# Kernel optimization log

Measured on AMD Instinct MI355X. Metric: run time of the kernel, lower is better.

## Reference

```python
import jax, jax.numpy as jnp
import numpy as np

SHOT, WAY, DIM, Q, R = 5, 32, 640, 4096, 10
TEMP, L, DIV = 16.0, 2.0, 10.0
EPS = 1e-5


def _expmap0(x, c):
    # x: (..., d); c: broadcastable to (..., 1). Exponential map at origin + ball projection.
    sc = jnp.sqrt(c)
    n = jnp.maximum(jnp.linalg.norm(x, axis=-1, keepdims=True), EPS)
    y = jnp.tanh(sc * n) * x / (sc * n)
    ny = jnp.maximum(jnp.linalg.norm(y, axis=-1, keepdims=True), EPS)
    maxn = (1.0 - 1e-3) / sc
    return jnp.where(ny > maxn, y * (maxn / ny), y)


def _dist(x, y, c):
    # Poincare distance: 2/sqrt(c) * artanh(sqrt(c) * ||mobius_add(-x, y)||)
    u = -x
    uy = jnp.sum(u * y, -1, keepdims=True)
    u2 = jnp.sum(u * u, -1, keepdims=True)
    y2 = jnp.sum(y * y, -1, keepdims=True)
    num = (1.0 + 2.0 * c * uy + c * y2) * u + (1.0 - c * u2) * y
    den = jnp.maximum(1.0 + 2.0 * c * uy + c * c * u2 * y2, EPS)
    n = jnp.linalg.norm(num / den, axis=-1, keepdims=True)
    sc = jnp.sqrt(c)
    arg = jnp.clip(sc * n, 0.0, 1.0 - EPS)
    return ((2.0 / sc) * jnp.arctanh(arg))[..., 0]


def setup_inputs() -> dict:
    key = jax.random.key(0)
    ks = jax.random.split(key, 8)
    f = lambda k, s: jax.random.normal(k, s, dtype=jnp.float32)
    z = lambda s: jnp.zeros(s, jnp.float32)
    return {
        "data_shot": f(ks[0], (SHOT * WAY, DIM)),
        "data_query": f(ks[1], (Q, DIM)),
        "W1": f(ks[2], (2 * DIM, 128)) * 0.05, "b1": z((128,)),
        "W2": f(ks[3], (128, 64)) * 0.05, "b2": z((64,)),
        "W3": f(ks[4], (64, 5)) * 0.05, "b3": z((5,)),
        "Wr1": f(ks[5], (2 * R + 2, R)) * 0.05, "br1": z((R,)),
        "Wr2": f(ks[6], (R, R + 1)) * 0.05, "br2": z((R + 1,)),
    }


def reference(data_shot, data_query, W1, b1, W2, b2, W3, b3, Wr1, br1, Wr2, br2):
    # --- episode stats + per-class curvature controller ---
    all_data = jnp.concatenate([data_shot, data_query], 0).mean(0)      # (dim,)
    protos = data_shot.reshape(SHOT, WAY, DIM).mean(0)                  # (way, dim)
    ctrl_in = jnp.concatenate([protos, jnp.broadcast_to(all_data, (WAY, DIM))], 1)
    h = jax.nn.relu(ctrl_in @ W1 + b1)
    h = jax.nn.relu(h @ W2 + b2)
    cand = jnp.arange(1, 6, dtype=jnp.float32) * (L / DIV)              # 5 curvature candidates
    c = jax.nn.softmax(h @ W3 + b3, axis=-1) @ cand                     # (way,) positive curvature

    # --- hyperbolic projection + per-class proto-query distances (vectorized over classes) ---
    proto_p = _expmap0(protos, c[:, None])                              # (way, dim)
    query_p = _expmap0(data_query[None], c[:, None, None])              # (way, Q, dim)
    dis_mat = _dist(proto_p[:, None, :], query_p, c[:, None, None])     # (way, Q)

    # --- sort + gather-based rerank features ---
    idx = jnp.argsort(dis_mat, axis=1)
    idx_near, idx_far = idx[:, :R], idx[:, R:]
    n_i_d = jnp.take_along_axis(dis_mat, idx_near, 1)                   # (way, R)
    o_i_d = jnp.take_along_axis(dis_mat, idx_far, 1).mean(1)            # (way,)
    dT = dis_mat.T                                                      # (Q, way)
    Gnear = dT[idx_near]                                                # (way, R, way): [i,k,j] = dis_mat[j, idx_near[i,k]]
    n_o_d = (Gnear.sum(-1) - n_i_d) / (WAY - 1)                         # (way, R)
    Gfar = dT[idx_far]                                                  # (way, Q-R, way)
    ii = jnp.arange(WAY)
    mlt = (ii[None, :] < ii[:, None]).astype(dis_mat.dtype)             # j < i
    mgt = (ii[None, :] > ii[:, None]).astype(dis_mat.dtype)             # j > i
    sumA = jnp.einsum('ikj,ij->i', Gfar, mlt)                           # gathered cols (rows before i)
    sumB = mgt @ dis_mat[:, R:].sum(1)                                  # raw cols R: (rows after i, as in source)
    o_o_d = (sumA + sumB) / ((WAY - 1) * (Q - R))

    # --- rerank controller MLP ---
    rr_in = jnp.concatenate([n_i_d, n_o_d, o_i_d[:, None], o_o_d[:, None]], 1)  # (way, 2R+2)
    hr = jax.nn.relu(rr_in @ Wr1 + br1)
    orr = hr @ Wr2 + br2                                                # (way, R+1)
    i_w = jax.nn.softmax(orr[:, :R], axis=-1)                           # (way, R)
    onw = jax.nn.sigmoid(orr[:, R])                                     # (way,)

    # --- proto update + final distances ---
    near_q = data_query[idx_near]                                       # (way, R, dim)
    wdq = (near_q * i_w[:, :, None]).sum(1)                             # (way, dim)
    tmp = protos * onw[:, None] + wdq * (1.0 - onw[:, None])
    test_proto = _expmap0(tmp, c[:, None])
    new_dis = _dist(test_proto[:, None, :], query_p, c[:, None, None])  # (way, Q)
    return -new_dis.T / TEMP                                            # (Q, way)
```

## Files before the change

### kernel.cpp

```cpp
#include <hip/hip_runtime.h>
#include <math.h>

#define NSHOT 5
#define WAY 32
#define DIM 640
#define NQ 4096
#define RNEAR 10

constexpr int OFF_PROTOS = 0;
constexpr int OFF_QPART  = 20480;
constexpr int OFF_C      = 102400;
constexpr int OFF_XVEC   = 102432;
constexpr int OFF_DIS    = 122912;
constexpr int OFF_S      = 253984;
constexpr int OFF_U      = 254016;
constexpr int OFF_NID    = 254048;
constexpr int OFF_TP     = 254368;
constexpr int OFF_NIDX   = 274848;
constexpr int OFF_Q2D    = 275200;
constexpr int OFF_X2D    = 283392;
constexpr int OFF_X2D2   = 283456;

__device__ __forceinline__ double wave_sum_d(double v) {
#pragma unroll
  for (int o = 32; o > 0; o >>= 1) v += __shfl_down(v, o, 64);
  return v;
}

__device__ __forceinline__ double dist_hyp(double c, double xdotq, double u2, double q2) {
  const double EPSd = 1e-5;
  double sc = sqrt(c);
  double nq = sqrt(q2);
  double nf = fmax(nq, EPSd);
  double th = tanh(sc * nf);
  double al = th / (sc * nf);
  double ny = fmax(al * nq, EPSd);
  double mx = 0.999 / sc;
  if (ny > mx) al *= mx / ny;
  double y2 = al * al * q2;
  double uy = -al * xdotq;
  double A = 1.0 + 2.0 * c * uy + c * y2;
  double B = 1.0 - c * u2;
  double den = fmax(1.0 + 2.0 * c * uy + c * c * u2 * y2, EPSd);
  double num2 = fmax(A * A * u2 + 2.0 * A * B * uy + B * B * y2, 0.0);
  double n = sqrt(num2) / den;
  double arg = sc * n;
  const double CLIP = (double)(1.0f - 1e-5f);
  arg = fmin(fmax(arg, 0.0), CLIP);
  return (1.0 / sc) * log((1.0 + arg) / (1.0 - arg));
}

__device__ __forceinline__ double expmap_scale(double c, double p2, double* u2out) {
  double sc = sqrt(c);
  double ntrue = sqrt(p2);
  double nf = fmax(ntrue, 1e-5);
  double th = tanh(sc * nf);
  double s0 = th / (sc * nf);
  double ny = fmax(s0 * ntrue, 1e-5);
  double mx = 0.999 / sc;
  if (ny > mx) s0 *= mx / ny;
  *u2out = s0 * s0 * p2;
  return s0;
}

__global__ __launch_bounds__(640) void k_fuse1(const float* __restrict__ Qm,
                                               const float* __restrict__ shot, float* ws) {
  __shared__ double q2w[32][10];
  int b = blockIdx.x, t = threadIdx.x;
  int lane = t & 63, wid = t >> 6;
  float protoval = 0.f;
  if (b < WAY) {
    float s = 0.f;
#pragma unroll
    for (int s5 = 0; s5 < NSHOT; ++s5) s += shot[(size_t)(s5 * WAY + b) * DIM + t];
    protoval = s * 0.2f;
    ws[OFF_PROTOS + b * DIM + t] = protoval;
  }
  int r0 = b * 32;
  float colacc = 0.f;
  for (int r = 0; r < 32; ++r) {
    float v = Qm[(size_t)(r0 + r) * DIM + t];
    colacc += v;
    double sq = (double)v * v;
    sq = wave_sum_d(sq);
    if (lane == 0) q2w[r][wid] = sq;
  }
  ws[OFF_QPART + b * DIM + t] = colacc + 5.f * protoval;
  __syncthreads();
  if (t < 32) {
    double s = 0.0;
#pragma unroll
    for (int k = 0; k < 10; ++k) s += q2w[t][k];
    ((double*)(ws + OFF_Q2D))[r0 + t] = s;
  }
}

__global__ __launch_bounds__(512) void k_ctrl(const float* __restrict__ W1, const float* __restrict__ b1,
                                              const float* __restrict__ W2, const float* __restrict__ b2,
                                              const float* __restrict__ W3, const float* __restrict__ b3,
                                              float* ws) {
  __shared__ float cat[2 * DIM];
  __shared__ float4 ampart[3][160];
  __shared__ float h1p[16][128];
  __shared__ float h1s[128];
  __shared__ float h2p[8][64], h2s[64];
  __shared__ float lg[5];
  __shared__ double redd[8];
  __shared__ double sBeta;
  int w = blockIdx.x, t = threadIdx.x;
  int lane = t & 63, wid = t >> 6;
  double ps = 0.0;
  for (int d = t; d < DIM; d += 512) {
    float v = ws[OFF_PROTOS + w * DIM + d];
    cat[d] = v; ps += (double)v * v;
  }
  ps = wave_sum_d(ps);
  if (lane == 0) redd[wid] = ps;
  if (t < 480) {
    int s = t / 160, quad = t - s * 160;
    int p0 = s * 43, p1 = (s == 2) ? 128 : (p0 + 43);
    float4 a = {0.f, 0.f, 0.f, 0.f};
#pragma unroll 4
    for (int p = p0; p < p1; ++p) {
      float4 v = *(const float4*)&ws[OFF_QPART + p * DIM + quad * 4];
      a.x += v.x; a.y += v.y; a.z += v.z; a.w += v.w;
    }
    ampart[s][quad] = a;
  }
  __syncthreads();
  if (t < 160) {
    float4 a = ampart[0][t], b4 = ampart[1][t], c4 = ampart[2][t];
    float4 r;
    r.x = (a.x + b4.x + c4.x) / 4256.f;
    r.y = (a.y + b4.y + c4.y) / 4256.f;
    r.z = (a.z + b4.z + c4.z) / 4256.f;
    r.w = (a.w + b4.w + c4.w) / 4256.f;
    *(float4*)&cat[DIM + t * 4] = r;
  }
  __syncthreads();
  {
    int ng = t & 31, ks = t >> 5;
    int k0 = ks * 80;
    float4 acc = {0.f, 0.f, 0.f, 0.f};
#pragma unroll 8
    for (int k = k0; k < k0 + 80; ++k) {
      float4 wr = *(const float4*)&W1[(size_t)k * 128 + ng * 4];
      float xv = cat[k];
      acc.x = fmaf(xv, wr.x, acc.x);
      acc.y = fmaf(xv, wr.y, acc.y);
      acc.z = fmaf(xv, wr.z, acc.z);
      acc.w = fmaf(xv, wr.w, acc.w);
    }
    *(float4*)&h1p[ks][ng * 4] = acc;
  }
  __syncthreads();
  if (t < 128) {
    float a = b1[t];
#pragma unroll
    for (int s = 0; s < 16; ++s) a += h1p[s][t];
    h1s[t] = fmaxf(a, 0.f);
  }
  __syncthreads();
  {
    int n = t & 63, s2 = t >> 6;
    int k0 = s2 * 16;
    float acc = 0.f;
#pragma unroll
    for (int k = 0; k < 16; ++k) acc = fmaf(h1s[k0 + k], W2[(size_t)(k0 + k) * 64 + n], acc);
    h2p[s2][n] = acc;
  }
  __syncthreads();
  if (t < 64) {
    float a = b2[t];
#pragma unroll
    for (int s = 0; s < 8; ++s) a += h2p[s][t];
    h2s[t] = fmaxf(a, 0.f);
  }
  __syncthreads();
  if (t < 5) {
    float a = b3[t];
    for (int k = 0; k < 64; ++k) a = fmaf(h2s[k], W3[k * 5 + t], a);
    lg[t] = a;
  }
  __syncthreads();
  if (t == 0) {
    double p2 = 0.0;
    for (int i = 0; i < 8; ++i) p2 += redd[i];
    double m = lg[0];
    for (int i = 1; i < 5; ++i) m = fmax(m, (double)lg[i]);
    double se = 0.0, cv = 0.0;
    for (int i = 0; i < 5; ++i) { double e = exp((double)lg[i] - m); se += e; cv += e * 0.2 * (double)(i + 1); }
    double c = cv / se;
    ws[OFF_C + w] = (float)c;
    double u2;
    sBeta = expmap_scale(c, p2, &u2);
    ((double*)(ws + OFF_X2D))[w] = u2;
  }
  __syncthreads();
  float beta = (float)sBeta;
  for (int d = t; d < DIM; d += 512) ws[OFF_XVEC + w * DIM + d] = beta * cat[d];
}

__global__ __launch_bounds__(256) void k_gemmdist(const float* __restrict__ X, const float* __restrict__ Qm,
                                                  float* __restrict__ ws, int mode, float* __restrict__ out) {
  __shared__ float S[2][40][68];
  int t = threadIdx.x;
  int q0 = blockIdx.x * 8;
  int rowA = t >> 4, quadA = t & 15;
  int rowB = (t + 256) >> 4;
  int rowC = (t + 512) >> 4;
  bool hasC = (t < 128);
  const float* srcA = (rowA < 8 ? Qm + (size_t)(q0 + rowA) * DIM : X + (size_t)(rowA - 8) * DIM) + quadA * 4;
  const float* srcB = X + (size_t)(rowB - 8) * DIM + quadA * 4;
  const float* srcC = X + (size_t)(rowC - 8) * DIM + quadA * 4;
  float4 pA = *(const float4*)srcA;
  float4 pB = *(const float4*)srcB;
  float4 pC = {0.f, 0.f, 0.f, 0.f};
  if (hasC) pC = *(const float4*)srcC;
  *(float4*)&S[0][rowA][quadA * 4] = pA;
  *(float4*)&S[0][rowB][quadA * 4] = pB;
  if (hasC) *(float4*)&S[0][rowC][quadA * 4] = pC;
  __syncthreads();
  int q = t & 7, w = t >> 3;
  float ax = 0.f, ay = 0.f, az = 0.f, aw = 0.f;
  for (int c = 0; c < 10; ++c) {
    int bsel = c & 1;
    if (c < 9) {
      size_t kc = (size_t)(c + 1) * 64;
      pA = *(const float4*)(srcA + kc);
      pB = *(const float4*)(srcB + kc);
      if (hasC) pC = *(const float4*)(srcC + kc);
    }
    const float* qr = &S[bsel][q][0];
    const float* xr = &S[bsel][8 + w][0];
#pragma unroll
    for (int kk = 0; kk < 64; kk += 4) {
      float4 qv = *(const float4*)(qr + kk);
      float4 xv = *(const float4*)(xr + kk);
      ax = fmaf(qv.x, xv.x, ax);
      ay = fmaf(qv.y, xv.y, ay);
      az = fmaf(qv.z, xv.z, az);
      aw = fmaf(qv.w, xv.w, aw);
    }
    if (c < 9) {
      __syncthreads();
      int nb = bsel ^ 1;
      *(float4*)&S[nb][rowA][quadA * 4] = pA;
      *(float4*)&S[nb][rowB][quadA * 4] = pB;
      if (hasC) *(float4*)&S[nb][rowC][quadA * 4] = pC;
      __syncthreads();
    }
  }
  float acc = (ax + ay) + (az + aw);
  const double* q2d   = (const double*)(ws + OFF_Q2D);
  const double* u2arr = (const double*)(ws + (mode ? OFF_X2D2 : OFF_X2D));
  int qq = q0 + q;
  double d = dist_hyp((double)ws[OFF_C + w], (double)acc, u2arr[w], q2d[qq]);
  if (mode == 0) {
    ws[OFF_DIS + (size_t)w * NQ + qq] = (float)d;
  } else {
    out[(size_t)qq * WAY + w] = (float)(-d / 16.0);
  }
}

__global__ __launch_bounds__(1024) void k_topk(float* ws, int* nidx) {
  __shared__ double sredS[16], sredU[16];
  __shared__ float wv[16]; __shared__ int wi[16];
  __shared__ int swi;
  int w = blockIdx.x, t = threadIdx.x;
  int lane = t & 63, wid = t >> 6;
  const float* base = ws + OFF_DIS + (size_t)w * NQ;
  float v0 = base[t], v1 = base[1024 + t], v2 = base[2048 + t], v3 = base[3072 + t];
  unsigned tk = 0;
  double s = (double)v0 + (double)v1 + (double)v2 + (double)v3;
  double u = (t < RNEAR) ? (double)v0 : 0.0;
  s = wave_sum_d(s);
  u = wave_sum_d(u);
  if (lane == 0) { sredS[wid] = s; sredU[wid] = u; }
  __syncthreads();
  if (t == 0) {
    double S = 0.0, U = 0.0;
    for (int k = 0; k < 16; ++k) { S += sredS[k]; U += sredU[k]; }
    ws[OFF_S + w] = (float)S;
    ws[OFF_U + w] = (float)U;
  }
  for (int r = 0; r < RNEAR; ++r) {
    float lv = INFINITY; int li = 0x7fffffff;
    if (!(tk & 1u) && (v0 < lv || (v0 == lv && t < li)))        { lv = v0; li = t; }
    if (!(tk & 2u) && (v1 < lv || (v1 == lv && 1024 + t < li))) { lv = v1; li = 1024 + t; }
    if (!(tk & 4u) && (v2 < lv || (v2 == lv && 2048 + t < li))) { lv = v2; li = 2048 + t; }
    if (!(tk & 8u) && (v3 < lv || (v3 == lv && 3072 + t < li))) { lv = v3; li = 3072 + t; }
#pragma unroll
    for (int o = 32; o > 0; o >>= 1) {
      float ov = __shfl_down(lv, o, 64);
      int oi = __shfl_down(li, o, 64);
      if (ov < lv || (ov == lv && oi < li)) { lv = ov; li = oi; }
    }
    if (lane == 0) { wv[wid] = lv; wi[wid] = li; }
    __syncthreads();
    if (t < 64) {
      float bv = (lane < 16) ? wv[lane] : INFINITY;
      int bi = (lane < 16) ? wi[lane] : 0x7fffffff;
#pragma unroll
      for (int o = 8; o > 0; o >>= 1) {
        float ov = __shfl_down(bv, o, 64);
        int oi = __shfl_down(bi, o, 64);
        if (ov < bv || (ov == bv && oi < bi)) { bv = ov; bi = oi; }
      }
      if (lane == 0) {
        ws[OFF_NID + w * RNEAR + r] = bv;
        nidx[w * RNEAR + r] = bi;
        swi = bi;
      }
    }
    __syncthreads();
    int sw = swi;
    if ((sw & 1023) == t) tk |= 1u << (sw >> 10);
  }
}

__global__ __launch_bounds__(512) void k_reftmp(const float* __restrict__ Qm,
                                                const float* __restrict__ Wr1, const float* __restrict__ br1,
                                                const float* __restrict__ Wr2, const float* __restrict__ br2,
                                                float* ws, const int* __restrict__ nidx) {
  __shared__ float colsh[RNEAR][33];
  __shared__ float rr[22];
  __shared__ float qjNid[RNEAR];
  __shared__ int qj[RNEAR];
  __shared__ float Ssh[WAY], Ush[WAY];
  __shared__ float hr[RNEAR], iw[RNEAR];
  __shared__ float onw_sh;
  __shared__ double p2red[8];
  __shared__ double gshd;
  int w = blockIdx.x, t = threadIdx.x;
  int lane = t & 63, wid = t >> 6;
  if (t < WAY) { Ssh[t] = ws[OFF_S + t]; Ush[t] = ws[OFF_U + t]; }
  if (t >= 64 && t < 64 + RNEAR) {
    int j = t - 64;
    qj[j] = nidx[w * RNEAR + j];
    qjNid[j] = ws[OFF_NID + w * RNEAR + j];
  }
  __syncthreads();
  if (t < WAY * RNEAR) {
    int j = t >> 5, w2 = t & 31;
    colsh[j][w2] = ws[OFF_DIS + (size_t)w2 * NQ + qj[j]];
  }
  __syncthreads();
  if (t < RNEAR) {
    double cs = 0.0, pc = 0.0;
    for (int w2 = 0; w2 < WAY; ++w2) {
      float dv = colsh[t][w2];
      cs += dv;
      if (w2 < w) pc += dv;
    }
    rr[t] = qjNid[t];
    rr[RNEAR + t] = (float)((cs - qjNid[t]) / (double)(WAY - 1));
    colsh[t][32] = (float)pc;
  }
  __syncthreads();
  if (t == 0) {
    double sn = 0.0; for (int j = 0; j < RNEAR; ++j) sn += rr[j];
    double oi = ((double)Ssh[w] - sn) / (double)(NQ - RNEAR);
    double pref = 0.0; for (int j = 0; j < w; ++j) pref += Ssh[j];
    double suf = 0.0; for (int j = w + 1; j < WAY; ++j) suf += (double)Ssh[j] - (double)Ush[j];
    double spc = 0.0; for (int j = 0; j < RNEAR; ++j) spc += colsh[j][32];
    rr[20] = (float)oi;
    rr[21] = (float)((pref - spc + suf) / ((double)(WAY - 1) * (double)(NQ - RNEAR)));
  }
  __syncthreads();
  if (t < RNEAR) {
    float a = br1[t];
    for (int k = 0; k < 22; ++k) a = fmaf(rr[k], Wr1[k * RNEAR + t], a);
    hr[t] = fmaxf(a, 0.f);
  }
  __syncthreads();
  if (t == 0) {
    double o[11];
    for (int r2 = 0; r2 < 11; ++r2) {
      float a = br2[r2];
      for (int k = 0; k < RNEAR; ++k) a = fmaf(hr[k], Wr2[k * 11 + r2], a);
      o[r2] = a;
    }
    double m = o[0]; for (int i = 1; i < RNEAR; ++i) m = fmax(m, o[i]);
    double se = 0.0; double e[RNEAR];
    for (int i = 0; i < RNEAR; ++i) { e[i] = exp(o[i] - m); se += e[i]; }
    for (int i = 0; i < RNEAR; ++i) iw[i] = (float)(e[i] / se);
    onw_sh = (float)(1.0 / (1.0 + exp(-o[10])));
  }
  __syncthreads();
  float onwv = onw_sh;
  float a0 = 0.f, a1 = 0.f;
  bool has2 = (t + 512 < DIM);
  double ls = 0.0;
  {
    int d = t;
    float wd = 0.f;
#pragma unroll
    for (int j = 0; j < RNEAR; ++j) wd = fmaf(Qm[(size_t)qj[j] * DIM + d], iw[j], wd);
    a0 = ws[OFF_PROTOS + w * DIM + d] * onwv + wd * (1.f - onwv);
    ls += (double)a0 * a0;
  }
  if (has2) {
    int d = t + 512;
    float wd = 0.f;
#pragma unroll
    for (int j = 0; j < RNEAR; ++j) wd = fmaf(Qm[(size_t)qj[j] * DIM + d], iw[j], wd);
    a1 = ws[OFF_PROTOS + w * DIM + d] * onwv + wd * (1.f - onwv);
    ls += (double)a1 * a1;
  }
  ls = wave_sum_d(ls);
  if (lane == 0) p2red[wid] = ls;
  __syncthreads();
  if (t == 0) {
    double p2 = 0.0;
    for (int i = 0; i < 8; ++i) p2 += p2red[i];
    double c = (double)ws[OFF_C + w];
    double u2;
    gshd = expmap_scale(c, p2, &u2);
    ((double*)(ws + OFF_X2D2))[w] = u2;
  }
  __syncthreads();
  float g = (float)gshd;
  ws[OFF_TP + w * DIM + t] = g * a0;
  if (has2) ws[OFF_TP + w * DIM + t + 512] = g * a1;
}

extern "C" void kernel_launch(void* const* d_in, const int* in_sizes, int n_in,
                              void* d_out, int out_size, void* d_ws, size_t ws_size,
                              hipStream_t stream) {
  (void)in_sizes; (void)n_in; (void)out_size; (void)ws_size;
  const float* shot = (const float*)d_in[0];
  const float* qry  = (const float*)d_in[1];
  const float* W1   = (const float*)d_in[2];
  const float* b1   = (const float*)d_in[3];
  const float* W2   = (const float*)d_in[4];
  const float* b2   = (const float*)d_in[5];
  const float* W3   = (const float*)d_in[6];
  const float* b3   = (const float*)d_in[7];
  const float* Wr1  = (const float*)d_in[8];
  const float* br1  = (const float*)d_in[9];
  const float* Wr2  = (const float*)d_in[10];
  const float* br2  = (const float*)d_in[11];
  float* ws = (float*)d_ws;
  float* out = (float*)d_out;
  int* nidx = (int*)(ws + OFF_NIDX);

  hipLaunchKernelGGL(k_fuse1,    dim3(128), dim3(640), 0, stream, qry, shot, ws);
  hipLaunchKernelGGL(k_ctrl,     dim3(32), dim3(512), 0, stream, W1, b1, W2, b2, W3, b3, ws);
  hipLaunchKernelGGL(k_gemmdist, dim3(512), dim3(256), 0, stream, ws + OFF_XVEC, qry, ws, 0, out);
  hipLaunchKernelGGL(k_topk,     dim3(32), dim3(1024), 0, stream, ws, nidx);
  hipLaunchKernelGGL(k_reftmp,   dim3(32), dim3(512), 0, stream, qry, Wr1, br1, Wr2, br2, ws, nidx);
  hipLaunchKernelGGL(k_gemmdist, dim3(512), dim3(256), 0, stream, ws + OFF_TP, qry, ws, 1, out);
}
```

Measured before the change: 85.72 us.

## Use per-wave top-k with a single merge and drop a redundant GEMM barrier

k_topk now has each wave select its own 10 nearest candidates with xor-shuffles and no block barriers between rounds. A single wave then merges the 160 candidates into the final top-10, replacing the two __syncthreads per round of the old scheme. This is correct because the global top-10 must lie in the union of the per-wave top-10s. Separately, the barrier before writing the prefetch buffer in the double-buffered distance loop is removed, since the end-of-iteration barrier already orders the reads of that buffer. The cost is a little extra shared memory and a serial merge pass.

```diff
diff --git a/kernel.cpp b/kernel.cpp
--- a/kernel.cpp
+++ b/kernel.cpp
@@ -243,7 +243,6 @@
       aw = fmaf(qv.w, xv.w, aw);
     }
     if (c < 9) {
-      __syncthreads();
       int nb = bsel ^ 1;
       *(float4*)&S[nb][rowA][quadA * 4] = pA;
       *(float4*)&S[nb][rowB][quadA * 4] = pB;
@@ -265,8 +264,8 @@
 
 __global__ __launch_bounds__(1024) void k_topk(float* ws, int* nidx) {
   __shared__ double sredS[16], sredU[16];
-  __shared__ float wv[16]; __shared__ int wi[16];
-  __shared__ int swi;
+  __shared__ float cval[160];
+  __shared__ int cidx[160];
   int w = blockIdx.x, t = threadIdx.x;
   int lane = t & 63, wid = t >> 6;
   const float* base = ws + OFF_DIS + (size_t)w * NQ;
@@ -277,13 +276,6 @@
   s = wave_sum_d(s);
   u = wave_sum_d(u);
   if (lane == 0) { sredS[wid] = s; sredU[wid] = u; }
-  __syncthreads();
-  if (t == 0) {
-    double S = 0.0, U = 0.0;
-    for (int k = 0; k < 16; ++k) { S += sredS[k]; U += sredU[k]; }
-    ws[OFF_S + w] = (float)S;
-    ws[OFF_U + w] = (float)U;
-  }
   for (int r = 0; r < RNEAR; ++r) {
     float lv = INFINITY; int li = 0x7fffffff;
     if (!(tk & 1u) && (v0 < lv || (v0 == lv && t < li)))        { lv = v0; li = t; }
@@ -292,30 +284,45 @@
     if (!(tk & 8u) && (v3 < lv || (v3 == lv && 3072 + t < li))) { lv = v3; li = 3072 + t; }
 #pragma unroll
     for (int o = 32; o > 0; o >>= 1) {
-      float ov = __shfl_down(lv, o, 64);
-      int oi = __shfl_down(li, o, 64);
+      float ov = __shfl_xor(lv, o, 64);
+      int oi = __shfl_xor(li, o, 64);
       if (ov < lv || (ov == lv && oi < li)) { lv = ov; li = oi; }
     }
-    if (lane == 0) { wv[wid] = lv; wi[wid] = li; }
-    __syncthreads();
-    if (t < 64) {
-      float bv = (lane < 16) ? wv[lane] : INFINITY;
-      int bi = (lane < 16) ? wi[lane] : 0x7fffffff;
-#pragma unroll
-      for (int o = 8; o > 0; o >>= 1) {
-        float ov = __shfl_down(bv, o, 64);
-        int oi = __shfl_down(bi, o, 64);
-        if (ov < bv || (ov == bv && oi < bi)) { bv = ov; bi = oi; }
+    if (lane == 0) { cval[wid * RNEAR + r] = lv; cidx[wid * RNEAR + r] = li; }
+    if ((li & 1023) == t) tk |= 1u << (li >> 10);
+  }
+  __syncthreads();
+  if (t == 0) {
+    double S = 0.0, U = 0.0;
+    for (int k = 0; k < 16; ++k) { S += sredS[k]; U += sredU[k]; }
+    ws[OFF_S + w] = (float)S;
+    ws[OFF_U + w] = (float)U;
+  }
+  if (t < 64) {
+    float c0 = cval[t], c1 = cval[t + 64];
+    int i0 = cidx[t], i1 = cidx[t + 64];
+    float c2 = (t < 32) ? cval[t + 128] : INFINITY;
+    int i2 = (t < 32) ? cidx[t + 128] : 0x7fffffff;
+    unsigned m = 0;
+    for (int r = 0; r < RNEAR; ++r) {
+      float lv = INFINITY; int li = 0x7fffffff;
+      if (!(m & 1u) && (c0 < lv || (c0 == lv && i0 < li))) { lv = c0; li = i0; }
+      if (!(m & 2u) && (c1 < lv || (c1 == lv && i1 < li))) { lv = c1; li = i1; }
+      if (!(m & 4u) && (c2 < lv || (c2 == lv && i2 < li))) { lv = c2; li = i2; }
+#pragma unroll
+      for (int o = 32; o > 0; o >>= 1) {
+        float ov = __shfl_xor(lv, o, 64);
+        int oi = __shfl_xor(li, o, 64);
+        if (ov < lv || (ov == lv && oi < li)) { lv = ov; li = oi; }
       }
       if (lane == 0) {
-        ws[OFF_NID + w * RNEAR + r] = bv;
-        nidx[w * RNEAR + r] = bi;
-        swi = bi;
+        ws[OFF_NID + w * RNEAR + r] = lv;
+        nidx[w * RNEAR + r] = li;
       }
-    }
-    __syncthreads();
-    int sw = swi;
-    if ((sw & 1023) == t) tk |= 1u << (sw >> 10);
+      if (i0 == li) m |= 1u;
+      if (i1 == li) m |= 2u;
+      if (i2 == li) m |= 4u;
+    }
   }
 }
 
```

New measurement: 86.85 us. Within noise of the previous version (+1.3%).
